# Kernel optimization log

Measured on AMD Instinct MI355X. Metric: run time of the kernel, lower is better.

The kernel has to match this reference:

```python
import math
import jax, jax.numpy as jnp
import numpy as np

DIM, HEADS, HD = 384, 12, 32
FEAT, WIN, SHIFT = (64, 64), (8, 8), (4, 4)
L = WIN[0] * WIN[1]  # window area = 64
MAX_LOGIT = math.log(1.0 / 0.01)


def _rel_log_coords():
    # pair-wise relative positions, log-spaced (static, numpy)
    coords = np.stack(np.meshgrid(np.arange(WIN[0]), np.arange(WIN[1]), indexing='ij'), 0).reshape(2, -1)
    rel = (coords[:, :, None] - coords[:, None, :]).transpose(1, 2, 0).reshape(-1, 2).astype(np.float32)
    return np.sign(rel) * np.log1p(np.abs(rel))  # [L*L, 2]


def _attn_mask():
    # shifted-window attention mask (static, numpy): 9 regions -> -100 across regions
    H, W = FEAT
    img = np.zeros((H, W), np.int32)
    cnt = 0
    for h0, h1 in ((0, H - WIN[0]), (H - WIN[0], H - SHIFT[0]), (H - SHIFT[0], H)):
        for w0, w1 in ((0, W - WIN[1]), (W - WIN[1], W - SHIFT[1]), (W - SHIFT[1], W)):
            img[h0:h1, w0:w1] = cnt
            cnt += 1
    mw = img.reshape(H // WIN[0], WIN[0], W // WIN[1], WIN[1]).transpose(0, 2, 1, 3).reshape(-1, L)
    diff = mw[:, None, :] - mw[:, :, None]
    return np.where(diff != 0, -100.0, 0.0).astype(np.float32)  # [nW, L, L]


def _ln(x, w, b, eps=1e-5):
    mu = x.mean(-1, keepdims=True)
    var = ((x - mu) ** 2).mean(-1, keepdims=True)
    return (x - mu) / jnp.sqrt(var + eps) * w + b


def setup_inputs() -> dict:
    key = jax.random.key(0)
    ks = jax.random.split(key, 12)
    B = 32
    s = 0.02
    return {
        'x': jax.random.normal(ks[0], (B, FEAT[0], FEAT[1], DIM), jnp.float32),
        'qkv_w': jax.random.normal(ks[1], (3 * DIM, DIM), jnp.float32) * s,
        'qkv_b': jnp.zeros((3 * DIM,), jnp.float32),
        'proj_w': jax.random.normal(ks[2], (DIM, DIM), jnp.float32) * s,
        'proj_b': jnp.zeros((DIM,), jnp.float32),
        'meta_w1': jax.random.normal(ks[3], (384, 2), jnp.float32) * 0.1,
        'meta_b1': jnp.zeros((384,), jnp.float32),
        'meta_w2': jax.random.normal(ks[4], (HEADS, 384), jnp.float32) * 0.1,
        'meta_b2': jnp.zeros((HEADS,), jnp.float32),
        'logit_scale': jnp.full((HEADS,), math.log(10.0), jnp.float32),
        'norm1_w': jnp.ones((DIM,), jnp.float32),
        'norm1_b': jnp.zeros((DIM,), jnp.float32),
        'fc1_w': jax.random.normal(ks[5], (4 * DIM, DIM), jnp.float32) * s,
        'fc1_b': jnp.zeros((4 * DIM,), jnp.float32),
        'fc2_w': jax.random.normal(ks[6], (DIM, 4 * DIM), jnp.float32) * s,
        'fc2_b': jnp.zeros((DIM,), jnp.float32),
        'norm2_w': jnp.ones((DIM,), jnp.float32),
        'norm2_b': jnp.zeros((DIM,), jnp.float32),
    }


def reference(x, qkv_w, qkv_b, proj_w, proj_b, meta_w1, meta_b1, meta_w2, meta_b2,
              logit_scale, norm1_w, norm1_b, fc1_w, fc1_b, fc2_w, fc2_b, norm2_w, norm2_b):
    B, H, W, C = x.shape
    wh, ww = WIN
    # cyclic shift + window partition: (B,H,W,C) -> (B*nW, L, C)
    sx = jnp.roll(x, (-SHIFT[0], -SHIFT[1]), axis=(1, 2))
    xw = sx.reshape(B, H // wh, wh, W // ww, ww, C).transpose(0, 1, 3, 2, 4, 5).reshape(-1, L, C)
    Bw = xw.shape[0]
    qkv = (xw @ qkv_w.T + qkv_b).reshape(Bw, L, 3, HEADS, HD).transpose(2, 0, 3, 1, 4)
    q, k, v = qkv[0], qkv[1], qkv[2]  # [Bw, heads, L, hd]
    # cosine attention
    qn = q / jnp.maximum(jnp.linalg.norm(q, axis=-1, keepdims=True), 1e-12)
    kn = k / jnp.maximum(jnp.linalg.norm(k, axis=-1, keepdims=True), 1e-12)
    attn = jnp.einsum('bhqd,bhkd->bhqk', qn, kn)
    scale = jnp.exp(jnp.minimum(logit_scale, MAX_LOGIT)).reshape(1, HEADS, 1, 1)
    # MLP-based relative position bias
    rel = jnp.asarray(_rel_log_coords())
    bias = jax.nn.relu(rel @ meta_w1.T + meta_b1) @ meta_w2.T + meta_b2  # [L*L, heads]
    bias = bias.T.reshape(HEADS, L, L)
    attn = attn * scale + bias[None]
    # shift mask
    mask = jnp.asarray(_attn_mask())  # [nW, L, L]
    nW = mask.shape[0]
    attn = attn.reshape(Bw // nW, nW, HEADS, L, L) + mask[None, :, None]
    attn = jax.nn.softmax(attn.reshape(Bw, HEADS, L, L), axis=-1)
    out = jnp.einsum('bhqk,bhkd->bhqd', attn, v).transpose(0, 2, 1, 3).reshape(Bw, L, C)
    out = out @ proj_w.T + proj_b
    # window reverse + reverse shift
    out = out.reshape(B, H // wh, W // ww, wh, ww, C).transpose(0, 1, 3, 2, 4, 5).reshape(B, H, W, C)
    out = jnp.roll(out, (SHIFT[0], SHIFT[1]), axis=(1, 2))
    # post-norm residuals (SwinV2Cr style)
    x = x + _ln(out, norm1_w, norm1_b)
    h = jax.nn.gelu(x @ fc1_w.T + fc1_b, approximate=False) @ fc2_w.T + fc2_b
    x = x + _ln(h, norm2_w, norm2_b)
    return x
```

## Files before the change

kernel.cpp:

```cpp
#include <hip/hip_runtime.h>
#include <hip/hip_bf16.h>

typedef __attribute__((ext_vector_type(4))) float f32x4;
typedef __attribute__((ext_vector_type(4))) unsigned int u32x4;
typedef __attribute__((ext_vector_type(8))) __bf16 bf16x8;

#define DEV static __device__ __forceinline__

DEV unsigned short f2bf(float f) {
  unsigned u = __builtin_bit_cast(unsigned, f);
  u += 0x7fffu + ((u >> 16) & 1u);
  return (unsigned short)(u >> 16);
}
DEV float bf2f(unsigned short b) {
  return __builtin_bit_cast(float, ((unsigned)b) << 16);
}
DEV unsigned pk2(float a, float b) {
  return (unsigned)f2bf(a) | ((unsigned)f2bf(b) << 16);
}
DEV unsigned cvtpk(float lo, float hi) {
  unsigned r;
  asm("v_cvt_pk_bf16_f32 %0, %1, %2" : "=v"(r) : "v"(lo), "v"(hi));
  return r;
}
DEV float fexp2(float x) {
  float r;
  asm("v_exp_f32 %0, %1" : "=v"(r) : "v"(x));
  return r;
}
DEV f32x4 mfma16(u32x4 a, u32x4 b, f32x4 c) {
  return __builtin_amdgcn_mfma_f32_16x16x32_bf16(
      __builtin_bit_cast(bf16x8, a), __builtin_bit_cast(bf16x8, b), c, 0, 0, 0);
}
DEV float ssq8(u32x4 c) {
  float s = 0.f;
#pragma unroll
  for (int e = 0; e < 4; e++) {
    float lo = __builtin_bit_cast(float, c[e] << 16);
    float hi = __builtin_bit_cast(float, c[e] & 0xffff0000u);
    s += lo * lo + hi * hi;
  }
  return s;
}
DEV void gload16(const unsigned short* g, unsigned short* l) {
  __builtin_amdgcn_global_load_lds(
      (const __attribute__((address_space(1))) unsigned int*)g,
      (__attribute__((address_space(3))) unsigned int*)l, 16, 0, 0);
}

template <int EPI>
__global__ __launch_bounds__(512, 2) void gemm8(
    const unsigned short* __restrict__ A, const unsigned short* __restrict__ B,
    const float* __restrict__ bias, unsigned short* __restrict__ C,
    int Nc, int K, int nblocks) {
  __shared__ __align__(16) unsigned char smem[131072];
  unsigned short* As0 = (unsigned short*)smem;
  unsigned short* Bs0 = (unsigned short*)(smem + 65536);
  const int bid = blockIdx.x;
  const int mchunk = (gridDim.x >> 3) / nblocks;
  const int xcd = bid & 7, idx = bid >> 3;
  const int nb = idx % nblocks, ml = idx / nblocks;
  const int m0 = (xcd * mchunk + ml) * 256, n0 = nb * 256;
  const int tid = threadIdx.x, w = tid >> 6, l = tid & 63;
  const int lr = l & 15, lg = l >> 4;
  const int wm = (w >> 2) * 128, wn = (w & 3) * 64;
  const int srow = l >> 3;
  const int scol = ((l & 7) ^ srow) * 8;
  const int NT = K >> 6;

  auto stA = [&](int p, int kt, int half, int j) {
    int r = half * 128 + w * 16 + j * 8;
    gload16(A + (size_t)(m0 + r + srow) * K + kt * 64 + scol,
            As0 + p * 16384 + r * 64);
  };
  auto stB = [&](int p, int kt, int half, int j) {
    int r = half * 128 + w * 16 + j * 8;
    gload16(B + (size_t)(n0 + r + srow) * K + kt * 64 + scol,
            Bs0 + p * 16384 + r * 64);
  };

  const f32x4 z4 = {0.f, 0.f, 0.f, 0.f};
  f32x4 acc[8][4];
#pragma unroll
  for (int i = 0; i < 8; i++)
#pragma unroll
    for (int j = 0; j < 4; j++) acc[i][j] = z4;
  u32x4 af[8], bf[8];

#pragma unroll
  for (int ktp = 0; ktp < 2; ktp++) {
    stB(ktp, ktp, 0, 0); stB(ktp, ktp, 0, 1);
    stB(ktp, ktp, 1, 0); stB(ktp, ktp, 1, 1);
    stA(ktp, ktp, 0, 0); stA(ktp, ktp, 0, 1);
    stA(ktp, ktp, 1, 0); stA(ktp, ktp, 1, 1);
  }

  for (int kt = 0; kt < NT; ++kt) {
    const int p = kt & 1;
    if (kt + 1 < NT) {
      asm volatile("s_waitcnt vmcnt(8)" ::: "memory");
    } else {
      asm volatile("s_waitcnt vmcnt(0)" ::: "memory");
    }
    __builtin_amdgcn_s_barrier();

#pragma unroll
    for (int ni = 0; ni < 4; ni++)
#pragma unroll
      for (int ks = 0; ks < 2; ks++) {
        int R = wn + ni * 16 + lr;
        bf[ni * 2 + ks] = *(const u32x4*)&Bs0[p * 16384 + R * 64 +
                                             (((ks * 4 + lg) ^ (lr & 7)) * 8)];
      }
#pragma unroll
    for (int mi = 0; mi < 4; mi++)
#pragma unroll
      for (int ks = 0; ks < 2; ks++) {
        int R = wm + mi * 16 + lr;
        af[mi * 2 + ks] = *(const u32x4*)&As0[p * 16384 + R * 64 +
                                              (((ks * 4 + lg) ^ (lr & 7)) * 8)];
      }
    asm volatile("s_waitcnt lgkmcnt(0)" ::: "memory");
    __builtin_amdgcn_sched_barrier(0);
    __builtin_amdgcn_s_setprio(1);
#pragma unroll
    for (int mi = 0; mi < 4; mi++)
#pragma unroll
      for (int ni = 0; ni < 2; ni++)
#pragma unroll
        for (int ks = 0; ks < 2; ks++)
          acc[mi][ni] = mfma16(bf[ni * 2 + ks], af[mi * 2 + ks], acc[mi][ni]);
    __builtin_amdgcn_s_setprio(0);
    __builtin_amdgcn_s_barrier();

    if (kt + 2 < NT) { stB(p, kt + 2, 0, 0); stB(p, kt + 2, 0, 1); }
    __builtin_amdgcn_s_setprio(1);
#pragma unroll
    for (int mi = 0; mi < 4; mi++)
#pragma unroll
      for (int ni = 0; ni < 2; ni++)
#pragma unroll
        for (int ks = 0; ks < 2; ks++)
          acc[mi][ni + 2] =
              mfma16(bf[(ni + 2) * 2 + ks], af[mi * 2 + ks], acc[mi][ni + 2]);
    __builtin_amdgcn_s_setprio(0);
    __builtin_amdgcn_s_barrier();

#pragma unroll
    for (int mi = 0; mi < 4; mi++)
#pragma unroll
      for (int ks = 0; ks < 2; ks++) {
        int R = wm + 64 + mi * 16 + lr;
        af[mi * 2 + ks] = *(const u32x4*)&As0[p * 16384 + R * 64 +
                                              (((ks * 4 + lg) ^ (lr & 7)) * 8)];
      }
    if (kt + 2 < NT) { stB(p, kt + 2, 1, 0); stB(p, kt + 2, 1, 1); }
    asm volatile("s_waitcnt lgkmcnt(0)" ::: "memory");
    __builtin_amdgcn_sched_barrier(0);
    __builtin_amdgcn_s_setprio(1);
#pragma unroll
    for (int mi = 0; mi < 4; mi++)
#pragma unroll
      for (int ni = 0; ni < 2; ni++)
#pragma unroll
        for (int ks = 0; ks < 2; ks++)
          acc[mi + 4][ni] =
              mfma16(bf[ni * 2 + ks], af[mi * 2 + ks], acc[mi + 4][ni]);
    __builtin_amdgcn_s_setprio(0);
    __builtin_amdgcn_s_barrier();

    if (kt + 2 < NT) {
      stA(p, kt + 2, 0, 0); stA(p, kt + 2, 0, 1);
      stA(p, kt + 2, 1, 0); stA(p, kt + 2, 1, 1);
    }
    __builtin_amdgcn_s_setprio(1);
#pragma unroll
    for (int mi = 0; mi < 4; mi++)
#pragma unroll
      for (int ni = 0; ni < 2; ni++)
#pragma unroll
        for (int ks = 0; ks < 2; ks++)
          acc[mi + 4][ni + 2] =
              mfma16(bf[(ni + 2) * 2 + ks], af[mi * 2 + ks], acc[mi + 4][ni + 2]);
    __builtin_amdgcn_s_setprio(0);
  }

  __builtin_amdgcn_s_barrier();
#pragma unroll
  for (int mh = 0; mh < 2; mh++)
#pragma unroll
    for (int mi = 0; mi < 4; mi++) {
      int mloc = wm + mh * 64 + mi * 16 + lr;
      int msw = mloc & 7;
#pragma unroll
      for (int ni = 0; ni < 4; ni++) {
        f32x4 v = acc[mh * 4 + mi][ni];
        f32x4 bv = *(const f32x4*)&bias[n0 + wn + ni * 16 + lg * 4];
#pragma unroll
        for (int r = 0; r < 4; r++) {
          float t = v[r] + bv[r];
          if (EPI == 1) t = 0.5f * t * (1.0f + erff(t * 0.70710678f));
          v[r] = t;
        }
        int nbyte = (wn + ni * 16 + lg * 4) * 2;
        int addr = mloc * 512 + ((((nbyte >> 4) ^ msw) << 4) | (nbyte & 8));
        *(uint2*)(smem + addr) = make_uint2(cvtpk(v[0], v[1]), cvtpk(v[2], v[3]));
      }
    }
  __syncthreads();
#pragma unroll
  for (int c = 0; c < 16; c++) {
    int m = w * 32 + c * 2 + (l >> 5);
    int h = l & 31;
    u32x4 v = *(const u32x4*)(smem + m * 512 + ((h ^ (m & 7)) << 4));
    int n = n0 + h * 8;
    if (n < Nc) *(u32x4*)&C[(size_t)(m0 + m) * Nc + n] = v;
  }
}

template <int MODE>
__global__ __launch_bounds__(512, 2) void gemm_ln8(
    const unsigned short* __restrict__ A, const unsigned short* __restrict__ Bw,
    const float* __restrict__ bias, const float* __restrict__ resf,
    const unsigned short* __restrict__ resb, const float* __restrict__ nw,
    const float* __restrict__ nb, unsigned short* __restrict__ outb,
    float* __restrict__ outf, int K) {
  __shared__ __align__(16) unsigned short As[2][128 * 64];
  __shared__ __align__(16) unsigned short Bs[2][384 * 64];
  const int bid = blockIdx.x;
  const int swz = (bid & 7) * (gridDim.x >> 3) + (bid >> 3);
  const int m0 = swz * 128;
  const int tid = threadIdx.x, w = tid >> 6, l = tid & 63;
  const int lr = l & 15, lg = l >> 4;
  const int wm = (w >> 2) * 64, wn = (w & 3) * 96;
  const int srow = l >> 3;
  const int scol = ((l & 7) ^ srow) * 8;
  const int NT = K >> 6;

  auto stA = [&](int p, int kt, int j) {
    int r = w * 16 + j * 8;
    gload16(A + (size_t)(m0 + r + srow) * K + kt * 64 + scol, &As[p][r * 64]);
  };
  auto stB = [&](int p, int kt, int part, int j) {
    int r = part * 192 + w * 24 + j * 8;
    gload16(Bw + (size_t)(r + srow) * K + kt * 64 + scol, &Bs[p][r * 64]);
  };

  const f32x4 z4 = {0.f, 0.f, 0.f, 0.f};
  f32x4 acc[4][6];
#pragma unroll
  for (int i = 0; i < 4; i++)
#pragma unroll
    for (int j = 0; j < 6; j++) acc[i][j] = z4;
  u32x4 af[8], bf[12];

#pragma unroll
  for (int ktp = 0; ktp < 2; ktp++) {
    stB(ktp, ktp, 0, 0); stB(ktp, ktp, 0, 1); stB(ktp, ktp, 0, 2);
    stB(ktp, ktp, 1, 0); stB(ktp, ktp, 1, 1); stB(ktp, ktp, 1, 2);
    stA(ktp, ktp, 0); stA(ktp, ktp, 1);
  }

  for (int kt = 0; kt < NT; ++kt) {
    const int p = kt & 1;
    if (kt + 1 < NT) {
      asm volatile("s_waitcnt vmcnt(8)" ::: "memory");
    } else {
      asm volatile("s_waitcnt vmcnt(0)" ::: "memory");
    }
    __builtin_amdgcn_s_barrier();

#pragma unroll
    for (int nj = 0; nj < 6; nj++)
#pragma unroll
      for (int ks = 0; ks < 2; ks++) {
        int R = wn + nj * 16 + lr;
        bf[nj * 2 + ks] =
            *(const u32x4*)&Bs[p][R * 64 + (((ks * 4 + lg) ^ (lr & 7)) * 8)];
      }
#pragma unroll
    for (int mi = 0; mi < 4; mi++)
#pragma unroll
      for (int ks = 0; ks < 2; ks++) {
        int R = wm + mi * 16 + lr;
        af[mi * 2 + ks] =
            *(const u32x4*)&As[p][R * 64 + (((ks * 4 + lg) ^ (lr & 7)) * 8)];
      }
    asm volatile("s_waitcnt lgkmcnt(0)" ::: "memory");
    __builtin_amdgcn_sched_barrier(0);
    __builtin_amdgcn_s_setprio(1);
#pragma unroll
    for (int mi = 0; mi < 4; mi++)
#pragma unroll
      for (int nj = 0; nj < 2; nj++)
#pragma unroll
        for (int ks = 0; ks < 2; ks++)
          acc[mi][nj] = mfma16(af[mi * 2 + ks], bf[nj * 2 + ks], acc[mi][nj]);
    __builtin_amdgcn_s_setprio(0);
    __builtin_amdgcn_s_barrier();

    if (kt + 2 < NT) {
      stB(p, kt + 2, 0, 0); stB(p, kt + 2, 0, 1); stB(p, kt + 2, 0, 2);
    }
    __builtin_amdgcn_s_setprio(1);
#pragma unroll
    for (int mi = 0; mi < 4; mi++)
#pragma unroll
      for (int nj = 2; nj < 4; nj++)
#pragma unroll
        for (int ks = 0; ks < 2; ks++)
          acc[mi][nj] = mfma16(af[mi * 2 + ks], bf[nj * 2 + ks], acc[mi][nj]);
    __builtin_amdgcn_s_setprio(0);
    __builtin_amdgcn_s_barrier();

    if (kt + 2 < NT) {
      stB(p, kt + 2, 1, 0); stB(p, kt + 2, 1, 1); stB(p, kt + 2, 1, 2);
      stA(p, kt + 2, 0); stA(p, kt + 2, 1);
    }
    __builtin_amdgcn_s_setprio(1);
#pragma unroll
    for (int mi = 0; mi < 4; mi++)
#pragma unroll
      for (int nj = 4; nj < 6; nj++)
#pragma unroll
        for (int ks = 0; ks < 2; ks++)
          acc[mi][nj] = mfma16(af[mi * 2 + ks], bf[nj * 2 + ks], acc[mi][nj]);
    __builtin_amdgcn_s_setprio(0);
  }

  __syncthreads();
  float bcol[6];
#pragma unroll
  for (int j = 0; j < 6; j++) bcol[j] = bias[wn + j * 16 + lr];
#pragma unroll
  for (int i = 0; i < 4; i++)
#pragma unroll
    for (int j = 0; j < 6; j++)
#pragma unroll
      for (int r = 0; r < 4; r++) acc[i][j][r] += bcol[j];

  float* psum = (float*)(&As[0][0]);
  float* psq  = (float*)(&As[0][1024]);
  const int wn4 = w & 3;
#pragma unroll
  for (int i = 0; i < 4; i++)
#pragma unroll
    for (int r = 0; r < 4; r++) {
      float s1 = 0.f, s2 = 0.f;
#pragma unroll
      for (int j = 0; j < 6; j++) {
        float v = acc[i][j][r];
        s1 += v;
        s2 += v * v;
      }
#pragma unroll
      for (int d = 1; d < 16; d <<= 1) {
        s1 += __shfl_xor(s1, d, 64);
        s2 += __shfl_xor(s2, d, 64);
      }
      if (lr == 0) {
        int row = wm + i * 16 + lg * 4 + r;
        psum[wn4 * 128 + row] = s1;
        psq[wn4 * 128 + row] = s2;
      }
    }
  __syncthreads();

  float wcol[6], b2col[6];
#pragma unroll
  for (int j = 0; j < 6; j++) {
    int col = wn + j * 16 + lr;
    wcol[j] = nw[col];
    b2col[j] = nb[col];
  }
#pragma unroll
  for (int i = 0; i < 4; i++)
#pragma unroll
    for (int r = 0; r < 4; r++) {
      int row = wm + i * 16 + lg * 4 + r;
      float sum = psum[row] + psum[128 + row] + psum[256 + row] + psum[384 + row];
      float sq = psq[row] + psq[128 + row] + psq[256 + row] + psq[384 + row];
      float mu = sum * (1.f / 384.f);
      float rstd = rsqrtf(sq * (1.f / 384.f) - mu * mu + 1e-5f);
      size_t nbase;
      if (MODE == 0) {
        int mrow = m0 + row;
        int bb = mrow >> 12, widx = (mrow >> 6) & 63, tt = mrow & 63;
        int yy = (((widx >> 3) << 3) + (tt >> 3) + 4) & 63;
        int xx = (((widx & 7) << 3) + (tt & 7) + 4) & 63;
        nbase = (size_t)((bb << 12) | (yy << 6) | xx) * 384;
      } else {
        nbase = (size_t)(m0 + row) * 384;
      }
#pragma unroll
      for (int j = 0; j < 6; j++) {
        int col = wn + j * 16 + lr;
        float v = (acc[i][j][r] - mu) * rstd * wcol[j] + b2col[j];
        if (MODE == 0) {
          outb[nbase + col] = f2bf(resf[nbase + col] + v);
        } else {
          outf[nbase + col] = bf2f(resb[nbase + col]) + v;
        }
      }
    }
}

__global__ __launch_bounds__(256) void gather_cvt(
    const float* __restrict__ x, unsigned short* __restrict__ xb) {
  int wv = threadIdx.x >> 6, l = threadIdx.x & 63;
  int m = blockIdx.x * 4 + wv;
  int w = m >> 6, t = m & 63;
  int b = w >> 6, wy = (w >> 3) & 7, wx = w & 7;
  int oy = (wy * 8 + (t >> 3) + 4) & 63;
  int ox = (wx * 8 + (t & 7) + 4) & 63;
  const float2* src =
      (const float2*)(x + (size_t)((((b << 6) | oy) << 6) | ox) * 384 + l * 6);
  float2 f0 = src[0], f1 = src[1], f2 = src[2];
  unsigned* dst = (unsigned*)(xb + (size_t)m * 384 + l * 6);
  dst[0] = pk2(f0.x, f0.y);
  dst[1] = pk2(f1.x, f1.y);
  dst[2] = pk2(f2.x, f2.y);
}

__global__ __launch_bounds__(256, 4) void attn_win(
    const unsigned short* __restrict__ qkv, const float* __restrict__ btab2,
    const float* __restrict__ lscale, unsigned short* __restrict__ aout) {
  __shared__ __align__(16) unsigned short vT[4][32 * 72];
  __shared__ __align__(16) float rnk[4][64];
  const int w = blockIdx.x;
  const int wv = threadIdx.x >> 6, l = threadIdx.x & 63;
  const int h = blockIdx.y * 4 + wv;
  const int lr = l & 15, lg = l >> 4;
  const size_t base = (size_t)w * 64 * 1152 + h * 32;
  const f32x4 z4 = {0.f, 0.f, 0.f, 0.f};

  {
    const u32x4* vp = (const u32x4*)(qkv + base + (size_t)l * 1152 + 768);
#pragma unroll
    for (int c4 = 0; c4 < 4; c4++) {
      u32x4 c = vp[c4];
#pragma unroll
      for (int e = 0; e < 4; e++) {
        vT[wv][(c4 * 8 + e * 2) * 72 + l] = (unsigned short)(c[e] & 0xffffu);
        vT[wv][(c4 * 8 + e * 2 + 1) * 72 + l] = (unsigned short)(c[e] >> 16);
      }
    }
  }
  u32x4 kf[4];
#pragma unroll
  for (int tj = 0; tj < 4; tj++) {
    kf[tj] = *(const u32x4*)(qkv + base + (size_t)(tj * 16 + lr) * 1152 + 384 + lg * 8);
    float s = ssq8(kf[tj]);
    s += __shfl_xor(s, 16, 64);
    s += __shfl_xor(s, 32, 64);
    if (lg == 0) rnk[wv][tj * 16 + lr] = rsqrtf(fmaxf(s, 1e-24f));
  }
  u32x4 qf[4];
  float rnq[4];
#pragma unroll
  for (int ti = 0; ti < 4; ti++) {
    qf[ti] = *(const u32x4*)(qkv + base + (size_t)(ti * 16 + lr) * 1152 + lg * 8);
    float s = ssq8(qf[ti]);
    s += __shfl_xor(s, 16, 64);
    s += __shfl_xor(s, 32, 64);
    rnq[ti] = rsqrtf(fmaxf(s, 1e-24f));
  }
  __syncthreads();

  u32x4 vb[2][2];
#pragma unroll
  for (int kc = 0; kc < 2; kc++)
#pragma unroll
    for (int tj2 = 0; tj2 < 2; tj2++)
      vb[kc][tj2] = *(const u32x4*)(&vT[wv][(tj2 * 16 + lr) * 72 + kc * 32 + lg * 8]);

  const float scl2 = expf(fminf(lscale[h], 4.6051702f)) * 1.44269504f;
  const int wt = ((((w >> 3) & 7) == 7) ? 2 : 0) | (((w & 7) == 7) ? 1 : 0);
  const float* tabh = btab2 + (((size_t)wt * 12 + h) << 12);
  const int s0l = lr + ((l & 16) ? 32 : 0);
  const int s1l = s0l + 16;
  const bool hi = (l & 32) != 0;

#pragma unroll
  for (int ti = 0; ti < 4; ti++) {
    f32x4 sv[4];
#pragma unroll
    for (int tj = 0; tj < 4; tj++) sv[tj] = mfma16(kf[tj], qf[ti], z4);
    const float* tab = tabh + ((ti * 16 + lr) << 6);
    const float cb = rnq[ti] * scl2;
    f32x4 val[4];
    float m = -1e30f;
#pragma unroll
    for (int tj = 0; tj < 4; tj++) {
      f32x4 rk4 = *(const f32x4*)(&rnk[wv][tj * 16 + lg * 4]);
      f32x4 t4 = *(const f32x4*)(tab + tj * 16 + lg * 4);
#pragma unroll
      for (int r = 0; r < 4; r++) {
        float v = sv[tj][r] * (cb * rk4[r]) + t4[r];
        val[tj][r] = v;
        m = fmaxf(m, v);
      }
    }
    m = fmaxf(m, __shfl_xor(m, 16, 64));
    m = fmaxf(m, __shfl_xor(m, 32, 64));
    float den = 0.f;
#pragma unroll
    for (int tj = 0; tj < 4; tj++)
#pragma unroll
      for (int r = 0; r < 4; r++) {
        float p = fexp2(val[tj][r] - m);
        val[tj][r] = p;
        den += p;
      }
    den += __shfl_xor(den, 16, 64);
    den += __shfl_xor(den, 32, 64);
    float rden = 1.f / den;
#pragma unroll
    for (int tj = 0; tj < 4; tj++)
#pragma unroll
      for (int r = 0; r < 4; r++) val[tj][r] *= rden;

    f32x4 o[2] = {z4, z4};
#pragma unroll
    for (int kc = 0; kc < 2; kc++) {
      unsigned yA0 = cvtpk(val[2 * kc][0], val[2 * kc][1]);
      unsigned yA1 = cvtpk(val[2 * kc][2], val[2 * kc][3]);
      unsigned yB0 = cvtpk(val[2 * kc + 1][0], val[2 * kc + 1][1]);
      unsigned yB1 = cvtpk(val[2 * kc + 1][2], val[2 * kc + 1][3]);
      unsigned a0 = __shfl((int)yA0, s0l, 64), b0 = __shfl((int)yB0, s0l, 64);
      unsigned a1 = __shfl((int)yA1, s0l, 64), b1 = __shfl((int)yB1, s0l, 64);
      unsigned a2 = __shfl((int)yA0, s1l, 64), b2 = __shfl((int)yB0, s1l, 64);
      unsigned a3 = __shfl((int)yA1, s1l, 64), b3 = __shfl((int)yB1, s1l, 64);
      u32x4 pa = {hi ? b0 : a0, hi ? b1 : a1, hi ? b2 : a2, hi ? b3 : a3};
#pragma unroll
      for (int tj2 = 0; tj2 < 2; tj2++) o[tj2] = mfma16(pa, vb[kc][tj2], o[tj2]);
    }
#pragma unroll
    for (int tj2 = 0; tj2 < 2; tj2++)
#pragma unroll
      for (int r = 0; r < 4; r++)
        aout[(size_t)(w * 64 + ti * 16 + lg * 4 + r) * 384 + h * 32 + tj2 * 16 + lr] =
            f2bf(o[tj2][r]);
  }
}

__global__ __launch_bounds__(256) void btab2_kernel(
    const float* __restrict__ w1, const float* __restrict__ b1,
    const float* __restrict__ w2, const float* __restrict__ b2,
    float* __restrict__ btab2) {
  int p = blockIdx.x * 256 + threadIdx.x;
  int i = p >> 6, j = p & 63;
  float dy = (float)((i >> 3) - (j >> 3));
  float dx = (float)((i & 7) - (j & 7));
  float r0 = (dy > 0.f ? 1.f : (dy < 0.f ? -1.f : 0.f)) * log1pf(fabsf(dy));
  float r1 = (dx > 0.f ? 1.f : (dx < 0.f ? -1.f : 0.f)) * log1pf(fabsf(dx));
  float acc[12];
#pragma unroll
  for (int hh = 0; hh < 12; hh++) acc[hh] = b2[hh];
  for (int c = 0; c < 384; c++) {
    float hv = w1[c * 2] * r0 + w1[c * 2 + 1] * r1 + b1[c];
    hv = fmaxf(hv, 0.f);
#pragma unroll
    for (int hh = 0; hh < 12; hh++) acc[hh] += hv * w2[hh * 384 + c];
  }
  bool ddy = ((i >> 3) >= 4) != ((j >> 3) >= 4);
  bool ddx = ((i & 7) >= 4) != ((j & 7) >= 4);
  const float L2E = 1.44269504f;
#pragma unroll
  for (int wt = 0; wt < 4; wt++) {
    float mask = ((((wt >> 1) != 0) && ddy) || (((wt & 1) != 0) && ddx)) ? -100.f : 0.f;
#pragma unroll
    for (int hh = 0; hh < 12; hh++)
      btab2[(((size_t)wt * 12 + hh) << 12) + p] = (acc[hh] + mask) * L2E;
  }
}

__global__ __launch_bounds__(256) void cvt_kernel(
    const float* __restrict__ s, unsigned short* __restrict__ d, int n) {
  int i = blockIdx.x * 256 + threadIdx.x;
  if (i < n) d[i] = f2bf(s[i]);
}

__global__ __launch_bounds__(256) void cvt_pad_kernel(
    const float* __restrict__ s, unsigned short* __restrict__ d, int n_src,
    int n_tot) {
  int i = blockIdx.x * 256 + threadIdx.x;
  if (i < n_tot) d[i] = (i < n_src) ? f2bf(s[i]) : (unsigned short)0;
}

__global__ __launch_bounds__(256) void pad_bias_kernel(
    const float* __restrict__ s, float* __restrict__ d) {
  int i = blockIdx.x * 256 + threadIdx.x;
  if (i < 1280) d[i] = (i < 1152) ? s[i] : 0.f;
}

extern "C" void kernel_launch(void* const* d_in, const int* in_sizes, int n_in,
                              void* d_out, int out_size, void* d_ws,
                              size_t ws_size, hipStream_t stream) {
  (void)in_sizes; (void)n_in; (void)out_size; (void)ws_size;
  const float* x      = (const float*)d_in[0];
  const float* qkv_w  = (const float*)d_in[1];
  const float* qkv_b  = (const float*)d_in[2];
  const float* proj_w = (const float*)d_in[3];
  const float* proj_b = (const float*)d_in[4];
  const float* mw1    = (const float*)d_in[5];
  const float* mb1    = (const float*)d_in[6];
  const float* mw2    = (const float*)d_in[7];
  const float* mb2    = (const float*)d_in[8];
  const float* lsc    = (const float*)d_in[9];
  const float* n1w    = (const float*)d_in[10];
  const float* n1b    = (const float*)d_in[11];
  const float* w1     = (const float*)d_in[12];
  const float* b1     = (const float*)d_in[13];
  const float* w2     = (const float*)d_in[14];
  const float* b2     = (const float*)d_in[15];
  const float* n2w    = (const float*)d_in[16];
  const float* n2b    = (const float*)d_in[17];

  char* ws = (char*)d_ws;
  unsigned short* wqb  = (unsigned short*)(ws + 0);
  unsigned short* wpb  = (unsigned short*)(ws + 1048576);
  unsigned short* w1b  = (unsigned short*)(ws + 1441792);
  unsigned short* w2b  = (unsigned short*)(ws + 2621440);
  float* qbp           = (float*)(ws + 3801088);
  float* btab2         = (float*)(ws + 3866624);
  unsigned short* xb   = (unsigned short*)(ws + 4718592);
  unsigned short* qkvb = (unsigned short*)(ws + 105381888);
  unsigned short* att  = (unsigned short*)(ws + 440926208);
  unsigned short* y1b  = xb;
  unsigned short* hb   = qkvb;
  float* yout = (float*)d_out;

  cvt_pad_kernel<<<dim3(1920), 256, 0, stream>>>(qkv_w, wqb, 442368, 491520);
  cvt_kernel<<<dim3(576), 256, 0, stream>>>(proj_w, wpb, 147456);
  cvt_kernel<<<dim3(2304), 256, 0, stream>>>(w1, w1b, 589824);
  cvt_kernel<<<dim3(2304), 256, 0, stream>>>(w2, w2b, 589824);
  pad_bias_kernel<<<dim3(5), 256, 0, stream>>>(qkv_b, qbp);
  btab2_kernel<<<dim3(16), 256, 0, stream>>>(mw1, mb1, mw2, mb2, btab2);
  gather_cvt<<<dim3(32768), 256, 0, stream>>>(x, xb);

  gemm8<0><<<dim3(2560), 512, 0, stream>>>(xb, wqb, qbp, qkvb, 1152, 384, 5);
  attn_win<<<dim3(2048, 3), 256, 0, stream>>>(qkvb, btab2, lsc, att);
  gemm_ln8<0><<<dim3(1024), 512, 0, stream>>>(
      att, wpb, proj_b, x, nullptr, n1w, n1b, y1b, nullptr, 384);
  gemm8<1><<<dim3(3072), 512, 0, stream>>>(y1b, w1b, b1, hb, 1536, 384, 6);
  gemm_ln8<1><<<dim3(1024), 512, 0, stream>>>(
      hb, w2b, b2, nullptr, y1b, n2w, n2b, nullptr, yout, 1536);
}
```

Measured before the change: 1.153 ms.

## Merge weight-conversion launches and use sigmoid-approximated GELU in fc1 epilogue

Merges the four weight-cast kernels and the bias-pad kernel into one prep kernel, which saves four launches. Separately, the exact erf-based GELU in the fc1 GEMM epilogue is replaced by the sigmoid approximation x*sigmoid(1.702x), built from a hardware exp2 and reciprocal. That makes the epilogue cheaper but departs from the reference's exact GELU (approximate=False), so the output carries extra numerical error.

Result: faster. 1.048 ms (-9.1%).

```diff
diff --git a/kernel.cpp b/kernel.cpp
--- a/kernel.cpp
+++ b/kernel.cpp
@@ -27,6 +27,10 @@
   float r;
   asm("v_exp_f32 %0, %1" : "=v"(r) : "v"(x));
   return r;
+}
+DEV float gelu_s(float x) {
+  float e = fexp2(-2.45562457f * x);
+  return x * __builtin_amdgcn_rcpf(1.f + e);
 }
 DEV f32x4 mfma16(u32x4 a, u32x4 b, f32x4 c) {
   return __builtin_amdgcn_mfma_f32_16x16x32_bf16(
@@ -199,7 +203,7 @@
 #pragma unroll
         for (int r = 0; r < 4; r++) {
           float t = v[r] + bv[r];
-          if (EPI == 1) t = 0.5f * t * (1.0f + erff(t * 0.70710678f));
+          if (EPI == 1) t = gelu_s(t);
           v[r] = t;
         }
         int nbyte = (wn + ni * 16 + lg * 4) * 2;
@@ -575,23 +579,28 @@
   }
 }
 
-__global__ __launch_bounds__(256) void cvt_kernel(
-    const float* __restrict__ s, unsigned short* __restrict__ d, int n) {
+__global__ __launch_bounds__(256) void prep_kernel(
+    const float* __restrict__ qkv_w, const float* __restrict__ proj_w,
+    const float* __restrict__ w1, const float* __restrict__ w2,
+    const float* __restrict__ qkv_b, unsigned short* __restrict__ wqb,
+    unsigned short* __restrict__ wpb, unsigned short* __restrict__ w1b,
+    unsigned short* __restrict__ w2b, float* __restrict__ qbp) {
   int i = blockIdx.x * 256 + threadIdx.x;
-  if (i < n) d[i] = f2bf(s[i]);
-}
-
-__global__ __launch_bounds__(256) void cvt_pad_kernel(
-    const float* __restrict__ s, unsigned short* __restrict__ d, int n_src,
-    int n_tot) {
-  int i = blockIdx.x * 256 + threadIdx.x;
-  if (i < n_tot) d[i] = (i < n_src) ? f2bf(s[i]) : (unsigned short)0;
-}
-
-__global__ __launch_bounds__(256) void pad_bias_kernel(
-    const float* __restrict__ s, float* __restrict__ d) {
-  int i = blockIdx.x * 256 + threadIdx.x;
-  if (i < 1280) d[i] = (i < 1152) ? s[i] : 0.f;
+  if (i < 491520) {
+    wqb[i] = (i < 442368) ? f2bf(qkv_w[i]) : (unsigned short)0;
+  } else if (i < 638976) {
+    int j = i - 491520;
+    wpb[j] = f2bf(proj_w[j]);
+  } else if (i < 1228800) {
+    int j = i - 638976;
+    w1b[j] = f2bf(w1[j]);
+  } else if (i < 1818624) {
+    int j = i - 1228800;
+    w2b[j] = f2bf(w2[j]);
+  } else if (i < 1819904) {
+    int j = i - 1818624;
+    qbp[j] = (j < 1152) ? qkv_b[j] : 0.f;
+  }
 }
 
 extern "C" void kernel_launch(void* const* d_in, const int* in_sizes, int n_in,
@@ -631,11 +640,8 @@
   unsigned short* hb   = qkvb;
   float* yout = (float*)d_out;
 
-  cvt_pad_kernel<<<dim3(1920), 256, 0, stream>>>(qkv_w, wqb, 442368, 491520);
-  cvt_kernel<<<dim3(576), 256, 0, stream>>>(proj_w, wpb, 147456);
-  cvt_kernel<<<dim3(2304), 256, 0, stream>>>(w1, w1b, 589824);
-  cvt_kernel<<<dim3(2304), 256, 0, stream>>>(w2, w2b, 589824);
-  pad_bias_kernel<<<dim3(5), 256, 0, stream>>>(qkv_b, qbp);
+  prep_kernel<<<dim3(7109), 256, 0, stream>>>(qkv_w, proj_w, w1, w2, qkv_b,
+                                              wqb, wpb, w1b, w2b, qbp);
   btab2_kernel<<<dim3(16), 256, 0, stream>>>(mw1, mb1, mw2, mb2, btab2);
   gather_cvt<<<dim3(32768), 256, 0, stream>>>(x, xb);
 
```
